# Performance work log

Measured on AMD Instinct MI355X. Metric: run time of the kernel, lower is better.

## Reference

```python
import jax, jax.numpy as jnp
import numpy as np


def _split_box(v):
    # BoxTensor.from_vector: split last dim into (min z, max Z)
    D = v.shape[-1] // 2
    return v[..., :D], v[..., D:]


def setup_inputs() -> dict:
    key = jax.random.key(0)
    k1, k2 = jax.random.split(key)
    men_embeds = jax.random.normal(k1, (256, 128), dtype=jnp.float32)
    all_en_embeds = jax.random.normal(k2, (20000, 128), dtype=jnp.float32)
    return {"men_embeds": men_embeds, "all_en_embeds": all_en_embeds}


def reference(men_embeds, all_en_embeds):
    # men boxes: [M, D] min/max ; entity boxes: [N, D] min/max
    zm, Zm = _split_box(men_embeds)
    ze, Ze = _split_box(all_en_embeds)
    # intersection box per (mention, candidate): [M, N, D]
    lo = jnp.maximum(zm[:, None, :], ze[None, :, :])
    hi = jnp.minimum(Zm[:, None, :], Ze[None, :, :])
    # soft volume: prod_d softplus(side) -> log-volume = sum log softplus
    log_int_vol = jnp.sum(jnp.log(jax.nn.softplus(hi - lo)), axis=-1)   # [M, N]
    log_men_vol = jnp.sum(jnp.log(jax.nn.softplus(Zm - zm)), axis=-1)   # [M]
    # containment log prob = log vol(men ∩ en) - log vol(men); logits = exp(.)
    return jnp.exp(log_int_vol - log_men_vol[:, None])
```

## Files before the change

### kernel.cpp

```cpp
#include <hip/hip_runtime.h>


#define BM 32
#define BN 64
#define DD 64
#define MST 34
#define NST 68
#define CLEN 8
#define NCHUNK 8

__global__ __launch_bounds__(256, 3)
void ivr_kernel(const float* __restrict__ men, const float* __restrict__ en,
                float* __restrict__ out, int M, int N) {
    __shared__ __align__(16) float sEm[DD][MST];
    __shared__ __align__(16) float sIm[DD][MST];
    __shared__ __align__(16) float sEe[DD][NST];
    __shared__ __align__(16) float sIe[DD][NST];
    __shared__ float sRc[NCHUNK][MST];

    const int tx = threadIdx.x;
    const int m0 = blockIdx.y * BM;
    const int n0 = blockIdx.x * BN;

    {
        const int m = tx >> 3;
        const int c = tx & 7;
        int mm = m0 + m; if (mm >= M) mm = M - 1;
        const float* row = men + (size_t)mm * 128;
        float prod = 1.0f;
        #pragma unroll
        for (int k = 0; k < CLEN; ++k) {
            const int d = c * CLEN + k;
            const float Em = __expf(row[DD + d]);
            const float Im = __expf(-row[d]);
            sEm[d][m] = Em;
            sIm[d][m] = Im;
            prod *= __log2f(1.0f + Em * Im);
        }
        sRc[c][m] = 1.0f / prod;
    }
    for (int i = tx; i < BN * DD; i += 256) {
        const int d = i & (DD - 1);
        const int n = i >> 6;
        int nn = n0 + n; if (nn >= N) nn = N - 1;
        sEe[d][n] = __expf(en[(size_t)nn * 128 + DD + d]);
        sIe[d][n] = __expf(-en[(size_t)nn * 128 + d]);
    }
    __syncthreads();

    const int ni = (tx & 15) * 4;
    const int mi = (tx >> 4) * 2;

    float p[2][4];
    #pragma unroll
    for (int i = 0; i < 2; ++i)
        #pragma unroll
        for (int j = 0; j < 4; ++j) p[i][j] = 1.0f;

    #pragma unroll 1
    for (int c = 0; c < NCHUNK; ++c) {
        #pragma unroll
        for (int k = 0; k < CLEN; ++k) {
            const int d = c * CLEN + k;
            const float2 Em2 = *reinterpret_cast<const float2*>(&sEm[d][mi]);
            const float2 Im2 = *reinterpret_cast<const float2*>(&sIm[d][mi]);
            const float4 Ee4 = *reinterpret_cast<const float4*>(&sEe[d][ni]);
            const float4 Ie4 = *reinterpret_cast<const float4*>(&sIe[d][ni]);
            const float EmA[2] = {Em2.x, Em2.y};
            const float ImA[2] = {Im2.x, Im2.y};
            const float EeA[4] = {Ee4.x, Ee4.y, Ee4.z, Ee4.w};
            const float IeA[4] = {Ie4.x, Ie4.y, Ie4.z, Ie4.w};
            #pragma unroll
            for (int i = 0; i < 2; ++i) {
                #pragma unroll
                for (int j = 0; j < 4; ++j) {
                    const float u = fminf(EmA[i], EeA[j]) * fminf(ImA[i], IeA[j]);
                    p[i][j] *= __log2f(1.0f + u);
                }
            }
        }
        const float rc0 = sRc[c][mi];
        const float rc1 = sRc[c][mi + 1];
        #pragma unroll
        for (int j = 0; j < 4; ++j) { p[0][j] *= rc0; p[1][j] *= rc1; }
    }

    #pragma unroll
    for (int i = 0; i < 2; ++i) {
        const int m = m0 + mi + i;
        if (m >= M) continue;
        const int n = n0 + ni;
        if (n + 4 <= N) {
            *reinterpret_cast<float4*>(&out[(size_t)m * N + n]) =
                make_float4(p[i][0], p[i][1], p[i][2], p[i][3]);
        } else {
            #pragma unroll
            for (int j = 0; j < 4; ++j)
                if (n + j < N) out[(size_t)m * N + n + j] = p[i][j];
        }
    }
}

extern "C" void kernel_launch(void* const* d_in, const int* in_sizes, int n_in,
                              void* d_out, int out_size, void* d_ws, size_t ws_size,
                              hipStream_t stream) {
    const float* men = (const float*)d_in[0];
    const float* en  = (const float*)d_in[1];
    float* out = (float*)d_out;
    const int M = in_sizes[0] / 128;
    const int N = in_sizes[1] / 128;
    dim3 grid((N + BN - 1) / BN, (M + BM - 1) / BM);
    ivr_kernel<<<grid, dim3(256), 0, stream>>>(men, en, out, M, N);
}
```

Before: 143.0 us.

## Enlarge mention tile to 64, use 4x4 thread tiles and split D into halves

Doubles the mention tile per block so each thread computes a 4x4 output micro-tile instead of 2x4. This halves the number of blocks and the redundant exp of entity rows per output. The feature dimension is now processed in two halves of 32, which shrinks shared memory to allow four blocks per CU. Global loads become float4-vectorised. In exchange there are more registers per thread, an extra barrier between halves, and fewer total blocks (313x4 instead of 313x8), which may reduce load balance.

```diff
diff --git a/kernel.cpp b/kernel.cpp
--- a/kernel.cpp
+++ b/kernel.cpp
@@ -1,102 +1,127 @@
 #include <hip/hip_runtime.h>
 
 
-#define BM 32
+#define BM 64
 #define BN 64
-#define DD 64
-#define MST 34
-#define NST 68
+#define DH 32
+#define ST 68
 #define CLEN 8
-#define NCHUNK 8
+#define NCH 4
 
-__global__ __launch_bounds__(256, 3)
+__global__ __launch_bounds__(256, 4)
 void ivr_kernel(const float* __restrict__ men, const float* __restrict__ en,
                 float* __restrict__ out, int M, int N) {
-    __shared__ __align__(16) float sEm[DD][MST];
-    __shared__ __align__(16) float sIm[DD][MST];
-    __shared__ __align__(16) float sEe[DD][NST];
-    __shared__ __align__(16) float sIe[DD][NST];
-    __shared__ float sRc[NCHUNK][MST];
+    __shared__ __align__(16) float sEm[DH][ST];
+    __shared__ __align__(16) float sIm[DH][ST];
+    __shared__ __align__(16) float sEe[DH][ST];
+    __shared__ __align__(16) float sIe[DH][ST];
+    __shared__ __align__(16) float sRc[NCH][ST];
 
     const int tx = threadIdx.x;
     const int m0 = blockIdx.y * BM;
     const int n0 = blockIdx.x * BN;
 
-    {
-        const int m = tx >> 3;
-        const int c = tx & 7;
-        int mm = m0 + m; if (mm >= M) mm = M - 1;
-        const float* row = men + (size_t)mm * 128;
-        float prod = 1.0f;
-        #pragma unroll
-        for (int k = 0; k < CLEN; ++k) {
-            const int d = c * CLEN + k;
-            const float Em = __expf(row[DD + d]);
-            const float Im = __expf(-row[d]);
-            sEm[d][m] = Em;
-            sIm[d][m] = Im;
-            prod *= __log2f(1.0f + Em * Im);
-        }
-        sRc[c][m] = 1.0f / prod;
-    }
-    for (int i = tx; i < BN * DD; i += 256) {
-        const int d = i & (DD - 1);
-        const int n = i >> 6;
-        int nn = n0 + n; if (nn >= N) nn = N - 1;
-        sEe[d][n] = __expf(en[(size_t)nn * 128 + DD + d]);
-        sIe[d][n] = __expf(-en[(size_t)nn * 128 + d]);
-    }
-    __syncthreads();
+    const int ni = (tx & 15) * 4;
+    const int mi = (tx >> 4) * 4;
+    const int sr = tx >> 2;
+    const int sc = tx & 3;
 
-    const int ni = (tx & 15) * 4;
-    const int mi = (tx >> 4) * 2;
+    int mm = m0 + sr; if (mm >= M) mm = M - 1;
+    int nn = n0 + sr; if (nn >= N) nn = N - 1;
+    const float* mrow = men + (size_t)mm * 128 + sc * CLEN;
+    const float* erow = en  + (size_t)nn * 128 + sc * CLEN;
 
-    float p[2][4];
+    float p[4][4];
     #pragma unroll
-    for (int i = 0; i < 2; ++i)
+    for (int i = 0; i < 4; ++i)
         #pragma unroll
         for (int j = 0; j < 4; ++j) p[i][j] = 1.0f;
 
     #pragma unroll 1
-    for (int c = 0; c < NCHUNK; ++c) {
-        #pragma unroll
-        for (int k = 0; k < CLEN; ++k) {
-            const int d = c * CLEN + k;
-            const float2 Em2 = *reinterpret_cast<const float2*>(&sEm[d][mi]);
-            const float2 Im2 = *reinterpret_cast<const float2*>(&sIm[d][mi]);
-            const float4 Ee4 = *reinterpret_cast<const float4*>(&sEe[d][ni]);
-            const float4 Ie4 = *reinterpret_cast<const float4*>(&sIe[d][ni]);
-            const float EmA[2] = {Em2.x, Em2.y};
-            const float ImA[2] = {Im2.x, Im2.y};
-            const float EeA[4] = {Ee4.x, Ee4.y, Ee4.z, Ee4.w};
-            const float IeA[4] = {Ie4.x, Ie4.y, Ie4.z, Ie4.w};
+    for (int h = 0; h < 2; ++h) {
+        if (h) __syncthreads();
+
+        {
+            const float* r = mrow + h * DH;
+            const float4 a0 = *reinterpret_cast<const float4*>(r);
+            const float4 a1 = *reinterpret_cast<const float4*>(r + 4);
+            const float4 b0 = *reinterpret_cast<const float4*>(r + 64);
+            const float4 b1 = *reinterpret_cast<const float4*>(r + 68);
+            const float zA[8] = {a0.x,a0.y,a0.z,a0.w,a1.x,a1.y,a1.z,a1.w};
+            const float ZA[8] = {b0.x,b0.y,b0.z,b0.w,b1.x,b1.y,b1.z,b1.w};
+            float prod = 1.0f;
             #pragma unroll
-            for (int i = 0; i < 2; ++i) {
+            for (int k = 0; k < CLEN; ++k) {
+                const int dl = sc * CLEN + k;
+                const float Em = __expf(ZA[k]);
+                const float Im = __expf(-zA[k]);
+                sEm[dl][sr] = Em;
+                sIm[dl][sr] = Im;
+                prod *= __log2f(1.0f + Em * Im);
+            }
+            sRc[sc][sr] = 1.0f / prod;
+        }
+        {
+            const float* r = erow + h * DH;
+            const float4 a0 = *reinterpret_cast<const float4*>(r);
+            const float4 a1 = *reinterpret_cast<const float4*>(r + 4);
+            const float4 b0 = *reinterpret_cast<const float4*>(r + 64);
+            const float4 b1 = *reinterpret_cast<const float4*>(r + 68);
+            const float zA[8] = {a0.x,a0.y,a0.z,a0.w,a1.x,a1.y,a1.z,a1.w};
+            const float ZA[8] = {b0.x,b0.y,b0.z,b0.w,b1.x,b1.y,b1.z,b1.w};
+            #pragma unroll
+            for (int k = 0; k < CLEN; ++k) {
+                const int dl = sc * CLEN + k;
+                sEe[dl][sr] = __expf(ZA[k]);
+                sIe[dl][sr] = __expf(-zA[k]);
+            }
+        }
+        __syncthreads();
+
+        #pragma unroll 1
+        for (int c = 0; c < NCH; ++c) {
+            #pragma unroll
+            for (int k = 0; k < CLEN; ++k) {
+                const int d = c * CLEN + k;
+                const float4 Em4 = *reinterpret_cast<const float4*>(&sEm[d][mi]);
+                const float4 Im4 = *reinterpret_cast<const float4*>(&sIm[d][mi]);
+                const float4 Ee4 = *reinterpret_cast<const float4*>(&sEe[d][ni]);
+                const float4 Ie4 = *reinterpret_cast<const float4*>(&sIe[d][ni]);
+                const float EmA[4] = {Em4.x, Em4.y, Em4.z, Em4.w};
+                const float ImA[4] = {Im4.x, Im4.y, Im4.z, Im4.w};
+                const float EeA[4] = {Ee4.x, Ee4.y, Ee4.z, Ee4.w};
+                const float IeA[4] = {Ie4.x, Ie4.y, Ie4.z, Ie4.w};
                 #pragma unroll
-                for (int j = 0; j < 4; ++j) {
-                    const float u = fminf(EmA[i], EeA[j]) * fminf(ImA[i], IeA[j]);
-                    p[i][j] *= __log2f(1.0f + u);
+                for (int i = 0; i < 4; ++i) {
+                    #pragma unroll
+                    for (int j = 0; j < 4; ++j) {
+                        const float u = fminf(EmA[i], EeA[j]) * fminf(ImA[i], IeA[j]);
+                        p[i][j] *= __log2f(1.0f + u);
+                    }
                 }
             }
+            const float4 rc4 = *reinterpret_cast<const float4*>(&sRc[c][mi]);
+            const float rcA[4] = {rc4.x, rc4.y, rc4.z, rc4.w};
+            #pragma unroll
+            for (int i = 0; i < 4; ++i) {
+                #pragma unroll
+                for (int j = 0; j < 4; ++j) p[i][j] *= rcA[i];
+            }
         }
-        const float rc0 = sRc[c][mi];
-        const float rc1 = sRc[c][mi + 1];
-        #pragma unroll
-        for (int j = 0; j < 4; ++j) { p[0][j] *= rc0; p[1][j] *= rc1; }
     }
 
     #pragma unroll
-    for (int i = 0; i < 2; ++i) {
+    for (int i = 0; i < 4; ++i) {
         const int m = m0 + mi + i;
         if (m >= M) continue;
         const int n = n0 + ni;
+        float* o = out + (size_t)m * N + n;
         if (n + 4 <= N) {
-            *reinterpret_cast<float4*>(&out[(size_t)m * N + n]) =
-                make_float4(p[i][0], p[i][1], p[i][2], p[i][3]);
+            *reinterpret_cast<float4*>(o) = make_float4(p[i][0], p[i][1], p[i][2], p[i][3]);
         } else {
             #pragma unroll
             for (int j = 0; j < 4; ++j)
-                if (n + j < N) out[(size_t)m * N + n + j] = p[i][j];
+                if (n + j < N) o[j] = p[i][j];
         }
     }
 }
```

Measured after the change: 183.1 us. 28.1% more time.

## Split feature dimension into two halves to halve shared memory and raise occupancy

Applied to the files above, without the earlier changes.

Stages the 64-wide box dimension into shared memory in two 32-wide halves, with a barrier between them, instead of all at once. This halves the per-block LDS footprint, and the launch bound rises from 3 to 5 blocks per CU so more waves can hide latency. The cost is an extra __syncthreads and less overlap between loading the second half and computing the first.

```diff
diff --git a/kernel.cpp b/kernel.cpp
--- a/kernel.cpp
+++ b/kernel.cpp
@@ -4,49 +4,29 @@
 #define BM 32
 #define BN 64
 #define DD 64
+#define DH 32
 #define MST 34
 #define NST 68
 #define CLEN 8
 #define NCHUNK 8
 
-__global__ __launch_bounds__(256, 3)
+__global__ __launch_bounds__(256, 5)
 void ivr_kernel(const float* __restrict__ men, const float* __restrict__ en,
                 float* __restrict__ out, int M, int N) {
-    __shared__ __align__(16) float sEm[DD][MST];
-    __shared__ __align__(16) float sIm[DD][MST];
-    __shared__ __align__(16) float sEe[DD][NST];
-    __shared__ __align__(16) float sIe[DD][NST];
+    __shared__ __align__(16) float sEm[DH][MST];
+    __shared__ __align__(16) float sIm[DH][MST];
+    __shared__ __align__(16) float sEe[DH][NST];
+    __shared__ __align__(16) float sIe[DH][NST];
     __shared__ float sRc[NCHUNK][MST];
 
     const int tx = threadIdx.x;
     const int m0 = blockIdx.y * BM;
     const int n0 = blockIdx.x * BN;
 
-    {
-        const int m = tx >> 3;
-        const int c = tx & 7;
-        int mm = m0 + m; if (mm >= M) mm = M - 1;
-        const float* row = men + (size_t)mm * 128;
-        float prod = 1.0f;
-        #pragma unroll
-        for (int k = 0; k < CLEN; ++k) {
-            const int d = c * CLEN + k;
-            const float Em = __expf(row[DD + d]);
-            const float Im = __expf(-row[d]);
-            sEm[d][m] = Em;
-            sIm[d][m] = Im;
-            prod *= __log2f(1.0f + Em * Im);
-        }
-        sRc[c][m] = 1.0f / prod;
-    }
-    for (int i = tx; i < BN * DD; i += 256) {
-        const int d = i & (DD - 1);
-        const int n = i >> 6;
-        int nn = n0 + n; if (nn >= N) nn = N - 1;
-        sEe[d][n] = __expf(en[(size_t)nn * 128 + DD + d]);
-        sIe[d][n] = __expf(-en[(size_t)nn * 128 + d]);
-    }
-    __syncthreads();
+    const int sm = tx >> 3;
+    const int c8 = tx & 7;
+    int mm = m0 + sm; if (mm >= M) mm = M - 1;
+    const float* mrow = men + (size_t)mm * 128;
 
     const int ni = (tx & 15) * 4;
     const int mi = (tx >> 4) * 2;
@@ -58,31 +38,61 @@
         for (int j = 0; j < 4; ++j) p[i][j] = 1.0f;
 
     #pragma unroll 1
-    for (int c = 0; c < NCHUNK; ++c) {
-        #pragma unroll
-        for (int k = 0; k < CLEN; ++k) {
-            const int d = c * CLEN + k;
-            const float2 Em2 = *reinterpret_cast<const float2*>(&sEm[d][mi]);
-            const float2 Im2 = *reinterpret_cast<const float2*>(&sIm[d][mi]);
-            const float4 Ee4 = *reinterpret_cast<const float4*>(&sEe[d][ni]);
-            const float4 Ie4 = *reinterpret_cast<const float4*>(&sIe[d][ni]);
-            const float EmA[2] = {Em2.x, Em2.y};
-            const float ImA[2] = {Im2.x, Im2.y};
-            const float EeA[4] = {Ee4.x, Ee4.y, Ee4.z, Ee4.w};
-            const float IeA[4] = {Ie4.x, Ie4.y, Ie4.z, Ie4.w};
+    for (int h = 0; h < 2; ++h) {
+        if (h) __syncthreads();
+
+        if ((c8 >> 2) == h) {
+            float prod = 1.0f;
             #pragma unroll
-            for (int i = 0; i < 2; ++i) {
+            for (int k = 0; k < CLEN; ++k) {
+                const int d  = c8 * CLEN + k;
+                const int dl = d & (DH - 1);
+                const float Em = __expf(mrow[DD + d]);
+                const float Im = __expf(-mrow[d]);
+                sEm[dl][sm] = Em;
+                sIm[dl][sm] = Im;
+                prod *= __log2f(1.0f + Em * Im);
+            }
+            sRc[c8][sm] = 1.0f / prod;
+        }
+        for (int i = tx; i < BN * DH; i += 256) {
+            const int dl = i & (DH - 1);
+            const int n = i >> 5;
+            int nn = n0 + n; if (nn >= N) nn = N - 1;
+            const int d = h * DH + dl;
+            sEe[dl][n] = __expf(en[(size_t)nn * 128 + DD + d]);
+            sIe[dl][n] = __expf(-en[(size_t)nn * 128 + d]);
+        }
+        __syncthreads();
+
+        #pragma unroll 1
+        for (int c = 0; c < NCHUNK / 2; ++c) {
+            #pragma unroll
+            for (int k = 0; k < CLEN; ++k) {
+                const int dl = c * CLEN + k;
+                const float2 Em2 = *reinterpret_cast<const float2*>(&sEm[dl][mi]);
+                const float2 Im2 = *reinterpret_cast<const float2*>(&sIm[dl][mi]);
+                const float4 Ee4 = *reinterpret_cast<const float4*>(&sEe[dl][ni]);
+                const float4 Ie4 = *reinterpret_cast<const float4*>(&sIe[dl][ni]);
+                const float EmA[2] = {Em2.x, Em2.y};
+                const float ImA[2] = {Im2.x, Im2.y};
+                const float EeA[4] = {Ee4.x, Ee4.y, Ee4.z, Ee4.w};
+                const float IeA[4] = {Ie4.x, Ie4.y, Ie4.z, Ie4.w};
                 #pragma unroll
-                for (int j = 0; j < 4; ++j) {
-                    const float u = fminf(EmA[i], EeA[j]) * fminf(ImA[i], IeA[j]);
-                    p[i][j] *= __log2f(1.0f + u);
+                for (int i = 0; i < 2; ++i) {
+                    #pragma unroll
+                    for (int j = 0; j < 4; ++j) {
+                        const float u = fminf(EmA[i], EeA[j]) * fminf(ImA[i], IeA[j]);
+                        p[i][j] *= __log2f(1.0f + u);
+                    }
                 }
             }
+            const int cg = h * (NCHUNK / 2) + c;
+            const float rc0 = sRc[cg][mi];
+            const float rc1 = sRc[cg][mi + 1];
+            #pragma unroll
+            for (int j = 0; j < 4; ++j) { p[0][j] *= rc0; p[1][j] *= rc1; }
         }
-        const float rc0 = sRc[c][mi];
-        const float rc1 = sRc[c][mi + 1];
-        #pragma unroll
-        for (int j = 0; j < 4; ++j) { p[0][j] *= rc0; p[1][j] *= rc1; }
     }
 
     #pragma unroll
```

Measured after the change: 176.4 us. +23.4%, slower.

## Widen N tile to 128 with 512 threads, interleave mention data, reduce denominator via shuffles

Applied to the files above, without the earlier changes.

Doubles the entity tile to 128 columns and the block to 512 threads. Mention exp terms are packed as float2 pairs so one float4 LDS read covers both rows. Loads use vectorized float4 global reads, and the mention-volume denominator is reduced with warp shuffles and applied once at the end instead of per chunk. The aim is less staging overhead and fewer shared loads per FLOP. The trade-offs are the loss of per-chunk rescaling, which may risk underflow, and possible bank conflicts because the shared arrays are no longer padded.

```diff
diff --git a/kernel.cpp b/kernel.cpp
--- a/kernel.cpp
+++ b/kernel.cpp
@@ -2,54 +2,66 @@
 
 
 #define BM 32
-#define BN 64
+#define BN 128
 #define DD 64
-#define MST 34
-#define NST 68
-#define CLEN 8
-#define NCHUNK 8
 
-__global__ __launch_bounds__(256, 3)
+#define FD(PIJ, EMc, IMc, EEc, IEc) PIJ *= __log2f(1.0f + fminf(EMc, EEc) * fminf(IMc, IEc));
+
+__global__ __launch_bounds__(512, 4)
 void ivr_kernel(const float* __restrict__ men, const float* __restrict__ en,
                 float* __restrict__ out, int M, int N) {
-    __shared__ __align__(16) float sEm[DD][MST];
-    __shared__ __align__(16) float sIm[DD][MST];
-    __shared__ __align__(16) float sEe[DD][NST];
-    __shared__ __align__(16) float sIe[DD][NST];
-    __shared__ float sRc[NCHUNK][MST];
+    __shared__ __align__(16) float2 sMen[DD][BM];
+    __shared__ __align__(16) float  sEe[DD][BN];
+    __shared__ __align__(16) float  sIe[DD][BN];
 
     const int tx = threadIdx.x;
     const int m0 = blockIdx.y * BM;
     const int n0 = blockIdx.x * BN;
 
+    float rden;
     {
-        const int m = tx >> 3;
-        const int c = tx & 7;
-        int mm = m0 + m; if (mm >= M) mm = M - 1;
-        const float* row = men + (size_t)mm * 128;
-        float prod = 1.0f;
-        #pragma unroll
-        for (int k = 0; k < CLEN; ++k) {
-            const int d = c * CLEN + k;
-            const float Em = __expf(row[DD + d]);
-            const float Im = __expf(-row[d]);
-            sEm[d][m] = Em;
-            sIm[d][m] = Im;
-            prod *= __log2f(1.0f + Em * Im);
-        }
-        sRc[c][m] = 1.0f / prod;
+        const int ml = tx >> 4;
+        const int dc = (tx & 15) * 4;
+        int mm = m0 + ml; if (mm >= M) mm = M - 1;
+        const float* r = men + (size_t)mm * 128 + dc;
+        const float4 z = *reinterpret_cast<const float4*>(r);
+        const float4 Z = *reinterpret_cast<const float4*>(r + 64);
+        float Em, Im, prod;
+        Em = __expf(Z.x); Im = __expf(-z.x); sMen[dc + 0][ml] = make_float2(Em, Im); prod  = __log2f(1.0f + Em * Im);
+        Em = __expf(Z.y); Im = __expf(-z.y); sMen[dc + 1][ml] = make_float2(Em, Im); prod *= __log2f(1.0f + Em * Im);
+        Em = __expf(Z.z); Im = __expf(-z.z); sMen[dc + 2][ml] = make_float2(Em, Im); prod *= __log2f(1.0f + Em * Im);
+        Em = __expf(Z.w); Im = __expf(-z.w); sMen[dc + 3][ml] = make_float2(Em, Im); prod *= __log2f(1.0f + Em * Im);
+        prod *= __shfl_xor(prod, 1);
+        prod *= __shfl_xor(prod, 2);
+        prod *= __shfl_xor(prod, 4);
+        prod *= __shfl_xor(prod, 8);
+        rden = 1.0f / prod;
     }
-    for (int i = tx; i < BN * DD; i += 256) {
-        const int d = i & (DD - 1);
-        const int n = i >> 6;
-        int nn = n0 + n; if (nn >= N) nn = N - 1;
-        sEe[d][n] = __expf(en[(size_t)nn * 128 + DD + d]);
-        sIe[d][n] = __expf(-en[(size_t)nn * 128 + d]);
+    {
+        const int nl = tx >> 2;
+        const int c4 = tx & 3;
+        int nn = n0 + nl; if (nn >= N) nn = N - 1;
+        const float* r = en + (size_t)nn * 128 + c4 * 16;
+#define ESTG4(I) { \
+        const float4 z_ = *reinterpret_cast<const float4*>(r + (I) * 4); \
+        const float4 Z_ = *reinterpret_cast<const float4*>(r + 64 + (I) * 4); \
+        const int d_ = c4 * 16 + (I) * 4; \
+        sEe[d_ + 0][nl] = __expf(Z_.x); sIe[d_ + 0][nl] = __expf(-z_.x); \
+        sEe[d_ + 1][nl] = __expf(Z_.y); sIe[d_ + 1][nl] = __expf(-z_.y); \
+        sEe[d_ + 2][nl] = __expf(Z_.z); sIe[d_ + 2][nl] = __expf(-z_.z); \
+        sEe[d_ + 3][nl] = __expf(Z_.w); sIe[d_ + 3][nl] = __expf(-z_.w); }
+        ESTG4(0) ESTG4(1) ESTG4(2) ESTG4(3)
+#undef ESTG4
     }
     __syncthreads();
 
-    const int ni = (tx & 15) * 4;
-    const int mi = (tx >> 4) * 2;
+    const int ni = (tx & 31) * 4;
+    const int mi = (tx >> 5) * 2;
+
+    const float oden = __shfl_xor(rden, 16);
+    const int hib = (tx >> 4) & 1;
+    const float rd0 = hib ? oden : rden;
+    const float rd1 = hib ? rden : oden;
 
     float p[2][4];
     #pragma unroll
@@ -58,32 +70,26 @@
         for (int j = 0; j < 4; ++j) p[i][j] = 1.0f;
 
     #pragma unroll 1
-    for (int c = 0; c < NCHUNK; ++c) {
+    for (int c = 0; c < 8; ++c) {
         #pragma unroll
-        for (int k = 0; k < CLEN; ++k) {
-            const int d = c * CLEN + k;
-            const float2 Em2 = *reinterpret_cast<const float2*>(&sEm[d][mi]);
-            const float2 Im2 = *reinterpret_cast<const float2*>(&sIm[d][mi]);
+        for (int k = 0; k < 8; ++k) {
+            const int d = c * 8 + k;
+            const float4 mf  = *reinterpret_cast<const float4*>(&sMen[d][mi]);
             const float4 Ee4 = *reinterpret_cast<const float4*>(&sEe[d][ni]);
             const float4 Ie4 = *reinterpret_cast<const float4*>(&sIe[d][ni]);
-            const float EmA[2] = {Em2.x, Em2.y};
-            const float ImA[2] = {Im2.x, Im2.y};
-            const float EeA[4] = {Ee4.x, Ee4.y, Ee4.z, Ee4.w};
-            const float IeA[4] = {Ie4.x, Ie4.y, Ie4.z, Ie4.w};
-            #pragma unroll
-            for (int i = 0; i < 2; ++i) {
-                #pragma unroll
-                for (int j = 0; j < 4; ++j) {
-                    const float u = fminf(EmA[i], EeA[j]) * fminf(ImA[i], IeA[j]);
-                    p[i][j] *= __log2f(1.0f + u);
-                }
-            }
+            FD(p[0][0], mf.x, mf.y, Ee4.x, Ie4.x)
+            FD(p[0][1], mf.x, mf.y, Ee4.y, Ie4.y)
+            FD(p[0][2], mf.x, mf.y, Ee4.z, Ie4.z)
+            FD(p[0][3], mf.x, mf.y, Ee4.w, Ie4.w)
+            FD(p[1][0], mf.z, mf.w, Ee4.x, Ie4.x)
+            FD(p[1][1], mf.z, mf.w, Ee4.y, Ie4.y)
+            FD(p[1][2], mf.z, mf.w, Ee4.z, Ie4.z)
+            FD(p[1][3], mf.z, mf.w, Ee4.w, Ie4.w)
         }
-        const float rc0 = sRc[c][mi];
-        const float rc1 = sRc[c][mi + 1];
-        #pragma unroll
-        for (int j = 0; j < 4; ++j) { p[0][j] *= rc0; p[1][j] *= rc1; }
     }
+
+    #pragma unroll
+    for (int j = 0; j < 4; ++j) { p[0][j] *= rd0; p[1][j] *= rd1; }
 
     #pragma unroll
     for (int i = 0; i < 2; ++i) {
@@ -110,5 +116,5 @@
     const int M = in_sizes[0] / 128;
     const int N = in_sizes[1] / 128;
     dim3 grid((N + BN - 1) / BN, (M + BM - 1) / BM);
-    ivr_kernel<<<grid, dim3(256), 0, stream>>>(men, en, out, M, N);
+    ivr_kernel<<<grid, dim3(512), 0, stream>>>(men, en, out, M, N);
 }
```

After: 136.0 us. 4.9% less time.
